# Performance work log

Measured on AMD Instinct MI355X. Metric: run time of the kernel, lower is better.

The kernel has to match this reference:

```python
import jax, jax.numpy as jnp
import numpy as np

B, P, Q, H = 8, 2048, 512, 1024


def setup_inputs() -> dict:
    key = jax.random.key(0)
    k1, k2, k3, k4, k5 = jax.random.split(key, 5)
    passage = jax.random.normal(k1, (B, P, H), dtype=jnp.float32)
    question = jax.random.normal(k2, (B, Q, H), dtype=jnp.float32)
    q_mask = jax.random.randint(k3, (B, Q), 0, 2, dtype=jnp.int32)
    # map_linear params (torch Linear: y = x @ W.T + b)
    bound = 1.0 / np.sqrt(H)
    map_W = jax.random.uniform(k4, (H, H), jnp.float32, -bound, bound)
    map_b = jax.random.uniform(k5, (H,), jnp.float32, -bound, bound)
    return {"passage": passage, "question": question, "q_mask": q_mask,
            "map_W": map_W, "map_b": map_b}


def reference(passage, question, q_mask, map_W, map_b):
    # scores: [B, P, Q]
    scores = jnp.einsum("bph,bqh->bpq", passage, question)
    mask = q_mask.astype(scores.dtype)[:, None, :]  # [B, 1, Q], broadcasts over P
    # multiplicative masked softmax + renormalize (memory_efficient=False path)
    a = jax.nn.softmax(scores * mask, axis=-1) * mask
    alpha = a / (jnp.sum(a, axis=-1, keepdims=True) + 1e-13)
    # attend: [B, P, H]
    out = jnp.einsum("bpq,bqh->bph", alpha, question)
    # fused linear + ReLU
    return jax.nn.relu(jnp.einsum("bph,oh->bpo", out, map_W) + map_b)
```

## Files before the change

kernel.cpp:

```cpp
#include <hip/hip_runtime.h>
#include <hip/hip_bf16.h>

typedef _Float16 f16;
typedef _Float16 f16x8 __attribute__((ext_vector_type(8)));
typedef _Float16 f16x4 __attribute__((ext_vector_type(4)));
typedef _Float16 f16x2 __attribute__((ext_vector_type(2)));
typedef float f32x4 __attribute__((ext_vector_type(4)));
typedef float f32x2 __attribute__((ext_vector_type(2)));

#define B_ 8
#define P_ 2048
#define Q_ 512
#define H_ 1024

__device__ __forceinline__ void gload_lds16(const void* g, void* l) {
  __builtin_amdgcn_global_load_lds(
      (const __attribute__((address_space(1))) void*)g,
      (__attribute__((address_space(3))) void*)l, 16, 0, 0);
}

__global__ __launch_bounds__(256) void k_cvt16(const float* __restrict__ x,
                                               f16* __restrict__ y, int n4) {
  int i = blockIdx.x * blockDim.x + threadIdx.x;
  int stride = gridDim.x * blockDim.x;
  for (; i < n4; i += stride) {
    f32x4 v = ((const f32x4*)x)[i];
    f16x4 h;
#pragma unroll
    for (int j = 0; j < 4; ++j) h[j] = (f16)v[j];
    ((f16x4*)y)[i] = h;
  }
}

__global__ __launch_bounds__(256) void k_transpose(const float* __restrict__ q,
                                                   f16* __restrict__ qT,
                                                   f16* __restrict__ q16) {
  __shared__ float t[64][65];
  int b = blockIdx.z;
  int h0 = blockIdx.x * 64, q0 = blockIdx.y * 64;
  int tid = threadIdx.x;
  int c4 = (tid & 15) * 4;
  int r16 = tid >> 4;
  const float* src = q + ((long)b * Q_ + q0) * H_ + h0;
  f16* d16 = q16 + ((long)b * Q_ + q0) * H_ + h0;
#pragma unroll
  for (int i = 0; i < 4; ++i) {
    int r = r16 + i * 16;
    f32x4 v = *(const f32x4*)(src + (long)r * H_ + c4);
    f16x4 s;
#pragma unroll
    for (int j = 0; j < 4; ++j) s[j] = (f16)v[j];
    *(f16x4*)(d16 + (long)r * H_ + c4) = s;
    t[c4 + 0][r] = v[0];
    t[c4 + 1][r] = v[1];
    t[c4 + 2][r] = v[2];
    t[c4 + 3][r] = v[3];
  }
  __syncthreads();
  f16* dst = qT + ((long)b * H_ + h0) * Q_ + q0;
#pragma unroll
  for (int i = 0; i < 4; ++i) {
    int hr = r16 + i * 16;
    f16x4 o;
#pragma unroll
    for (int j = 0; j < 4; ++j) o[j] = (f16)t[hr][c4 + j];
    *(f16x4*)(dst + (long)hr * Q_ + c4) = o;
  }
}

__global__ __launch_bounds__(512, 2) void k_score_softmax(
    const float* __restrict__ passage, const f16* __restrict__ q16,
    const int* __restrict__ qmask, f16* __restrict__ alpha) {
  constexpr int NT = H_ / 32;
  __shared__ __align__(16) f16 smem[2048 + 32768];

  int orig = blockIdx.x;
  int z = orig & 7;
  int row0 = (orig >> 3) * 32;

  int tid = threadIdx.x, wv = tid >> 6, lane = tid & 63;
  int fr = lane & 15, kq = lane >> 4;
  int wc = wv * 64;
  int swz = (kq ^ ((fr >> 1) & 3)) * 8;

  int arow = tid >> 4;
  int acol2 = (tid & 15) * 2;
  const float* gA = passage + ((long)(z * P_ + row0 + arow)) * H_ + acol2;
  int aw = arow * 32 + ((acol2 >> 3) ^ ((arow >> 1) & 3)) * 8 + (acol2 & 7);

  const f16* gB = q16 + ((long)(z * Q_ + (tid >> 2))) * H_ +
                  (((tid & 3) ^ ((tid >> 3) & 3)) * 8);

  auto stageB = [&](int t) {
    const f16* g = gB + t * 32;
    f16* l = smem + 2048 + (t & 1) * 16384 + wv * 512;
#pragma unroll
    for (int p = 0; p < 4; ++p)
      gload_lds16(g + (long)p * 128 * H_, l + p * 4096);
  };
  auto writeA = [&](int t, f32x2 av) {
    f16x2 h;
    h[0] = (f16)av[0];
    h[1] = (f16)av[1];
    *(f16x2*)(smem + (t & 1) * 1024 + aw) = h;
  };

  f32x4 acc[2][4] = {};
  f32x2 areg0, areg1;

  areg0 = *(const f32x2*)gA;
  stageB(0);
  areg1 = *(const f32x2*)(gA + 32);
  writeA(0, areg0);
  asm volatile("s_waitcnt vmcnt(1) lgkmcnt(0)" ::: "memory");
  __builtin_amdgcn_s_barrier();
  __builtin_amdgcn_sched_barrier(0);

#pragma unroll 2
  for (int t = 0; t < NT; ++t) {
    if (t + 1 < NT) stageB(t + 1);
    f16x8 af[2], bf[4];
    const f16* Ab = smem + (t & 1) * 1024;
    const f16* Bb = smem + 2048 + (t & 1) * 16384;
#pragma unroll
    for (int m = 0; m < 2; ++m)
      af[m] = *(const f16x8*)(Ab + (m * 16 + fr) * 32 + swz);
#pragma unroll
    for (int n = 0; n < 4; ++n)
      bf[n] = *(const f16x8*)(Bb + (wc + n * 16 + fr) * 32 + swz);
    if (t + 1 < NT)
      writeA(t + 1, ((t + 1) & 1) ? areg1 : areg0);
    if (t + 2 < NT) {
      f32x2 a = *(const f32x2*)(gA + (t + 2) * 32);
      if ((t + 2) & 1) areg1 = a; else areg0 = a;
    }
    __builtin_amdgcn_s_setprio(1);
#pragma unroll
    for (int m = 0; m < 2; ++m)
#pragma unroll
      for (int n = 0; n < 4; ++n)
        acc[m][n] = __builtin_amdgcn_mfma_f32_16x16x32_f16(af[m], bf[n],
                                                           acc[m][n], 0, 0, 0);
    __builtin_amdgcn_s_setprio(0);
    if (t < NT - 2)
      asm volatile("s_waitcnt vmcnt(1) lgkmcnt(0)" ::: "memory");
    else if (t == NT - 2)
      asm volatile("s_waitcnt vmcnt(0) lgkmcnt(0)" ::: "memory");
    if (t < NT - 1) {
      __builtin_amdgcn_s_barrier();
      __builtin_amdgcn_sched_barrier(0);
    }
  }

  __syncthreads();
  float* red = (float*)smem;
  float* red2 = red + 256;
  const int* qm = qmask + z * Q_;
  float mk[4];
#pragma unroll
  for (int n = 0; n < 4; ++n) mk[n] = (float)qm[wc + n * 16 + fr];

  int rb = (lane >> 4) * 4;
  float rmax[2][4];
#pragma unroll
  for (int m = 0; m < 2; ++m)
#pragma unroll
    for (int j = 0; j < 4; ++j) {
      float v = acc[m][0][j] * mk[0];
#pragma unroll
      for (int n = 1; n < 4; ++n) v = fmaxf(v, acc[m][n][j] * mk[n]);
      v = fmaxf(v, __shfl_xor(v, 1, 64));
      v = fmaxf(v, __shfl_xor(v, 2, 64));
      v = fmaxf(v, __shfl_xor(v, 4, 64));
      v = fmaxf(v, __shfl_xor(v, 8, 64));
      if (fr == 0) red[(rb + m * 16 + j) * 8 + wv] = v;
    }
  __syncthreads();
#pragma unroll
  for (int m = 0; m < 2; ++m)
#pragma unroll
    for (int j = 0; j < 4; ++j) {
      int r = rb + m * 16 + j;
      float v = red[r * 8];
#pragma unroll
      for (int w = 1; w < 8; ++w) v = fmaxf(v, red[r * 8 + w]);
      rmax[m][j] = v;
    }
#pragma unroll
  for (int m = 0; m < 2; ++m)
#pragma unroll
    for (int j = 0; j < 4; ++j) {
      float zs = 0.f, ss = 0.f;
#pragma unroll
      for (int n = 0; n < 4; ++n) {
        float e = expf(acc[m][n][j] * mk[n] - rmax[m][j]);
        acc[m][n][j] = e;
        zs += e;
        ss += e * mk[n];
      }
      zs += __shfl_xor(zs, 1, 64); ss += __shfl_xor(ss, 1, 64);
      zs += __shfl_xor(zs, 2, 64); ss += __shfl_xor(ss, 2, 64);
      zs += __shfl_xor(zs, 4, 64); ss += __shfl_xor(ss, 4, 64);
      zs += __shfl_xor(zs, 8, 64); ss += __shfl_xor(ss, 8, 64);
      if (fr == 0) {
        red2[((rb + m * 16 + j) * 8 + wv) * 2] = zs;
        red2[((rb + m * 16 + j) * 8 + wv) * 2 + 1] = ss;
      }
    }
  __syncthreads();
  f16* ap = alpha + ((long)(z * P_ + row0)) * Q_;
#pragma unroll
  for (int m = 0; m < 2; ++m)
#pragma unroll
    for (int j = 0; j < 4; ++j) {
      int r = rb + m * 16 + j;
      float Z = 0.f, Sm = 0.f;
#pragma unroll
      for (int w = 0; w < 8; ++w) {
        Z += red2[(r * 8 + w) * 2];
        Sm += red2[(r * 8 + w) * 2 + 1];
      }
      float inv = 1.0f / (Sm + 1e-13f * Z);
#pragma unroll
      for (int n = 0; n < 4; ++n)
        ap[(long)r * Q_ + wc + n * 16 + fr] = (f16)(acc[m][n][j] * mk[n] * inv);
    }
}

template <int EPI, int NT>
__global__ __launch_bounds__(512, 2) void k_gemm256(
    const f16* __restrict__ A, const f16* __restrict__ Bm,
    void* __restrict__ Cv, const float* __restrict__ bias, int N, int gx,
    int gy, long sA, long sB, long sC) {
  constexpr int K = NT * 32;
  __shared__ __align__(16) f16 smem[65536];

  int nwg = gridDim.x;
  int orig = blockIdx.x;
  int wg = (orig & 7) * (nwg >> 3) + (orig >> 3);
  int bx = wg % gx;
  int tt = wg / gx;
  int by = tt % gy;
  int z = tt / gy;
  int row0 = by * 256, col0 = bx * 256;
  A += z * sA;
  Bm += z * sB;

  int tid = threadIdx.x, wv = tid >> 6, lane = tid & 63;

  bool isA = wv < 4;
  int u0 = (wv & 3) * 4;
  int srow = u0 * 16 + (lane >> 2);
  int sclog = ((lane & 3) ^ ((lane >> 3) & 3)) * 8;
  const f16* sbaseG = isA ? A + (long)(row0 + srow) * K + sclog
                          : Bm + (long)(col0 + srow) * K + sclog;
  int sbaseL = (isA ? 0 : 8192) + u0 * 512;

  auto stage = [&](int tile) {
    const f16* g = sbaseG + (long)tile * 32;
    f16* l = smem + (tile & 3) * 16384 + sbaseL;
#pragma unroll
    for (int j = 0; j < 4; ++j) gload_lds16(g + (long)j * 16 * K, l + j * 512);
  };

  int wr = (wv >> 2) * 128, wc = (wv & 3) * 64;
  int fr = lane & 15, kq = lane >> 4;
  int swz = (kq ^ ((fr >> 1) & 3)) * 8 + fr * 32;

  f32x4 acc[8][4] = {};
  auto compute = [&](int t) {
    const f16* bufA = smem + (t & 3) * 16384;
    const f16* bufB = bufA + 8192;
    f16x8 af[8], bfr[4];
#pragma unroll
    for (int m = 0; m < 8; ++m)
      af[m] = *(const f16x8*)(bufA + (wr + m * 16) * 32 + swz);
#pragma unroll
    for (int n = 0; n < 4; ++n)
      bfr[n] = *(const f16x8*)(bufB + (wc + n * 16) * 32 + swz);
#pragma unroll
    for (int m = 0; m < 8; ++m)
#pragma unroll
      for (int n = 0; n < 4; ++n)
        acc[m][n] = __builtin_amdgcn_mfma_f32_16x16x32_f16(af[m], bfr[n],
                                                           acc[m][n], 0, 0, 0);
  };

  stage(0);
  stage(1);
  stage(2);
  asm volatile("s_waitcnt vmcnt(8)" ::: "memory");
  __builtin_amdgcn_s_barrier();
  __builtin_amdgcn_sched_barrier(0);
  for (int t = 0; t < NT - 3; ++t) {
    stage(t + 3);
    compute(t);
    asm volatile("s_waitcnt vmcnt(8)" ::: "memory");
    __builtin_amdgcn_s_barrier();
    __builtin_amdgcn_sched_barrier(0);
  }
  compute(NT - 3);
  asm volatile("s_waitcnt vmcnt(4)" ::: "memory");
  __builtin_amdgcn_s_barrier();
  __builtin_amdgcn_sched_barrier(0);
  compute(NT - 2);
  asm volatile("s_waitcnt vmcnt(0)" ::: "memory");
  __builtin_amdgcn_s_barrier();
  __builtin_amdgcn_sched_barrier(0);
  compute(NT - 1);

  int r0 = row0 + wr + (lane >> 4) * 4;
  int c0 = col0 + wc + fr;
  if constexpr (EPI == 1) {
    f16* C = (f16*)Cv + z * sC;
#pragma unroll
    for (int m = 0; m < 8; ++m)
#pragma unroll
      for (int n = 0; n < 4; ++n)
#pragma unroll
        for (int j = 0; j < 4; ++j)
          C[(long)(r0 + m * 16 + j) * N + c0 + n * 16] = (f16)acc[m][n][j];
  } else {
    float* C = (float*)Cv;
#pragma unroll
    for (int n = 0; n < 4; ++n) {
      float bv = bias[c0 + n * 16];
#pragma unroll
      for (int m = 0; m < 8; ++m)
#pragma unroll
        for (int j = 0; j < 4; ++j) {
          float v = acc[m][n][j] + bv;
          C[(long)(r0 + m * 16 + j) * N + c0 + n * 16] = fmaxf(v, 0.f);
        }
    }
  }
}

extern "C" void kernel_launch(void* const* d_in, const int* in_sizes, int n_in,
                              void* d_out, int out_size, void* d_ws,
                              size_t ws_size, hipStream_t stream) {
  const float* passage = (const float*)d_in[0];
  const float* question = (const float*)d_in[1];
  const int* qmask = (const int*)d_in[2];
  const float* mapW = (const float*)d_in[3];
  const float* mapb = (const float*)d_in[4];

  char* ws = (char*)d_ws;
  size_t off = 0;
  auto alloc = [&](size_t bytes) {
    void* p = ws + off;
    off += (bytes + 255) & ~(size_t)255;
    return p;
  };
  f16* q16 = (f16*)alloc((size_t)B_ * Q_ * H_ * 2);
  f16* qT = (f16*)alloc((size_t)B_ * H_ * Q_ * 2);
  f16* w16 = (f16*)alloc((size_t)H_ * H_ * 2);
  f16* alpha = (f16*)alloc((size_t)B_ * P_ * Q_ * 2);
  f16* O = (f16*)alloc((size_t)B_ * P_ * H_ * 2);

  k_cvt16<<<512, 256, 0, stream>>>(mapW, w16, H_ * H_ / 4);
  k_transpose<<<dim3(H_ / 64, Q_ / 64, B_), 256, 0, stream>>>(question, qT,
                                                              q16);

  k_score_softmax<<<512, 512, 0, stream>>>(passage, q16, qmask, alpha);

  k_gemm256<1, Q_ / 32><<<256, 512, 0, stream>>>(
      alpha, qT, O, nullptr, H_, H_ / 256, P_ / 256, (long)P_ * Q_,
      (long)H_ * Q_, (long)P_ * H_);

  k_gemm256<2, H_ / 32><<<256, 512, 0, stream>>>(
      O, w16, d_out, mapb, H_, H_ / 256, (B_ * P_) / 256, 0, 0, 0);
}
```

Measured before the change: 121.6 us.

## Split score GEMM and softmax into separate kernels with larger 128x256 tiles

```diff
diff --git a/kernel.cpp b/kernel.cpp
--- a/kernel.cpp
+++ b/kernel.cpp
@@ -4,9 +4,8 @@
 typedef _Float16 f16;
 typedef _Float16 f16x8 __attribute__((ext_vector_type(8)));
 typedef _Float16 f16x4 __attribute__((ext_vector_type(4)));
-typedef _Float16 f16x2 __attribute__((ext_vector_type(2)));
 typedef float f32x4 __attribute__((ext_vector_type(4)));
-typedef float f32x2 __attribute__((ext_vector_type(2)));
+typedef int i32x4 __attribute__((ext_vector_type(4)));
 
 #define B_ 8
 #define P_ 2048
@@ -68,83 +67,97 @@
   }
 }
 
-__global__ __launch_bounds__(512, 2) void k_score_softmax(
+__global__ __launch_bounds__(512, 2) void k_gemm1(
     const float* __restrict__ passage, const f16* __restrict__ q16,
-    const int* __restrict__ qmask, f16* __restrict__ alpha) {
+    float* __restrict__ S) {
   constexpr int NT = H_ / 32;
-  __shared__ __align__(16) f16 smem[2048 + 32768];
+  __shared__ __align__(16) f16 smem[40960];
 
   int orig = blockIdx.x;
-  int z = orig & 7;
-  int row0 = (orig >> 3) * 32;
+  int wg = (orig & 7) * 32 + (orig >> 3);
+  int bx = wg & 1, by = (wg >> 1) & 15, z = wg >> 5;
+  int row0 = by * 128, col0 = bx * 256;
 
   int tid = threadIdx.x, wv = tid >> 6, lane = tid & 63;
   int fr = lane & 15, kq = lane >> 4;
-  int wc = wv * 64;
+  int wr = (wv >> 2) * 64, wc = (wv & 3) * 64;
   int swz = (kq ^ ((fr >> 1) & 3)) * 8;
 
-  int arow = tid >> 4;
-  int acol2 = (tid & 15) * 2;
-  const float* gA = passage + ((long)(z * P_ + row0 + arow)) * H_ + acol2;
-  int aw = arow * 32 + ((acol2 >> 3) ^ ((arow >> 1) & 3)) * 8 + (acol2 & 7);
-
-  const f16* gB = q16 + ((long)(z * Q_ + (tid >> 2))) * H_ +
+  int ar = tid >> 2, ac = tid & 3;
+  const float* gA = passage + ((long)(z * P_ + row0 + ar)) * H_ + ac * 8;
+  int aw = ar * 32 + ((ac ^ ((ar >> 1) & 3)) * 8);
+
+  const f16* gB = q16 + ((long)(z * Q_ + col0 + (tid >> 2))) * H_ +
                   (((tid & 3) ^ ((tid >> 3) & 3)) * 8);
 
   auto stageB = [&](int t) {
     const f16* g = gB + t * 32;
-    f16* l = smem + 2048 + (t & 1) * 16384 + wv * 512;
-#pragma unroll
-    for (int p = 0; p < 4; ++p)
-      gload_lds16(g + (long)p * 128 * H_, l + p * 4096);
-  };
-  auto writeA = [&](int t, f32x2 av) {
-    f16x2 h;
-    h[0] = (f16)av[0];
-    h[1] = (f16)av[1];
-    *(f16x2*)(smem + (t & 1) * 1024 + aw) = h;
-  };
-
-  f32x4 acc[2][4] = {};
-  f32x2 areg0, areg1;
-
-  areg0 = *(const f32x2*)gA;
+    f16* l = smem + 8192 + (t & 3) * 8192 + wv * 512;
+    gload_lds16(g, l);
+    gload_lds16(g + (long)128 * H_, l + 4096);
+  };
+  auto writeA = [&](int t, f32x4 lo, f32x4 hi) {
+    f16x8 h;
+#pragma unroll
+    for (int j = 0; j < 4; ++j) {
+      h[j] = (f16)lo[j];
+      h[4 + j] = (f16)hi[j];
+    }
+    *(f16x8*)(smem + (t & 1) * 4096 + aw) = h;
+  };
+
+  f32x4 acc[4][4] = {};
+  f32x4 a0lo, a0hi, a1lo, a1hi;
+
+  a0lo = *(const f32x4*)(gA);
+  a0hi = *(const f32x4*)(gA + 4);
+  a1lo = *(const f32x4*)(gA + 32);
+  a1hi = *(const f32x4*)(gA + 36);
   stageB(0);
-  areg1 = *(const f32x2*)(gA + 32);
-  writeA(0, areg0);
-  asm volatile("s_waitcnt vmcnt(1) lgkmcnt(0)" ::: "memory");
+  stageB(1);
+  stageB(2);
+  writeA(0, a0lo, a0hi);
+  asm volatile("s_waitcnt vmcnt(4) lgkmcnt(0)" ::: "memory");
   __builtin_amdgcn_s_barrier();
   __builtin_amdgcn_sched_barrier(0);
 
-#pragma unroll 2
+#pragma unroll 4
   for (int t = 0; t < NT; ++t) {
-    if (t + 1 < NT) stageB(t + 1);
-    f16x8 af[2], bf[4];
-    const f16* Ab = smem + (t & 1) * 1024;
-    const f16* Bb = smem + 2048 + (t & 1) * 16384;
-#pragma unroll
-    for (int m = 0; m < 2; ++m)
-      af[m] = *(const f16x8*)(Ab + (m * 16 + fr) * 32 + swz);
+    if (t + 2 < NT) {
+      const float* g = gA + (t + 2) * 32;
+      if (t & 1) {
+        a1lo = *(const f32x4*)(g);
+        a1hi = *(const f32x4*)(g + 4);
+      } else {
+        a0lo = *(const f32x4*)(g);
+        a0hi = *(const f32x4*)(g + 4);
+      }
+    }
+    if (t + 3 < NT) stageB(t + 3);
+    f16x8 af[4], bf[4];
+    const f16* Ab = smem + (t & 1) * 4096;
+    const f16* Bb = smem + 8192 + (t & 3) * 8192;
+#pragma unroll
+    for (int m = 0; m < 4; ++m)
+      af[m] = *(const f16x8*)(Ab + (wr + m * 16 + fr) * 32 + swz);
 #pragma unroll
     for (int n = 0; n < 4; ++n)
       bf[n] = *(const f16x8*)(Bb + (wc + n * 16 + fr) * 32 + swz);
     if (t + 1 < NT)
-      writeA(t + 1, ((t + 1) & 1) ? areg1 : areg0);
-    if (t + 2 < NT) {
-      f32x2 a = *(const f32x2*)(gA + (t + 2) * 32);
-      if ((t + 2) & 1) areg1 = a; else areg0 = a;
-    }
+      writeA(t + 1, (t & 1) ? a0lo : a1lo, (t & 1) ? a0hi : a1hi);
     __builtin_amdgcn_s_setprio(1);
 #pragma unroll
-    for (int m = 0; m < 2; ++m)
+    for (int m = 0; m < 4; ++m)
 #pragma unroll
       for (int n = 0; n < 4; ++n)
         acc[m][n] = __builtin_amdgcn_mfma_f32_16x16x32_f16(af[m], bf[n],
                                                            acc[m][n], 0, 0, 0);
     __builtin_amdgcn_s_setprio(0);
-    if (t < NT - 2)
-      asm volatile("s_waitcnt vmcnt(1) lgkmcnt(0)" ::: "memory");
-    else if (t == NT - 2)
+    if (t <= NT - 4)
+      asm volatile("s_waitcnt vmcnt(6) lgkmcnt(0)" ::: "memory");
+    else if (t == NT - 3)
+      asm volatile("s_waitcnt vmcnt(4) lgkmcnt(0)" ::: "memory");
+    else
       asm volatile("s_waitcnt vmcnt(0) lgkmcnt(0)" ::: "memory");
     if (t < NT - 1) {
       __builtin_amdgcn_s_barrier();
@@ -152,79 +165,56 @@
     }
   }
 
-  __syncthreads();
-  float* red = (float*)smem;
-  float* red2 = red + 256;
-  const int* qm = qmask + z * Q_;
-  float mk[4];
-#pragma unroll
-  for (int n = 0; n < 4; ++n) mk[n] = (float)qm[wc + n * 16 + fr];
-
-  int rb = (lane >> 4) * 4;
-  float rmax[2][4];
-#pragma unroll
-  for (int m = 0; m < 2; ++m)
-#pragma unroll
-    for (int j = 0; j < 4; ++j) {
-      float v = acc[m][0][j] * mk[0];
-#pragma unroll
-      for (int n = 1; n < 4; ++n) v = fmaxf(v, acc[m][n][j] * mk[n]);
-      v = fmaxf(v, __shfl_xor(v, 1, 64));
-      v = fmaxf(v, __shfl_xor(v, 2, 64));
-      v = fmaxf(v, __shfl_xor(v, 4, 64));
-      v = fmaxf(v, __shfl_xor(v, 8, 64));
-      if (fr == 0) red[(rb + m * 16 + j) * 8 + wv] = v;
-    }
-  __syncthreads();
-#pragma unroll
-  for (int m = 0; m < 2; ++m)
-#pragma unroll
-    for (int j = 0; j < 4; ++j) {
-      int r = rb + m * 16 + j;
-      float v = red[r * 8];
-#pragma unroll
-      for (int w = 1; w < 8; ++w) v = fmaxf(v, red[r * 8 + w]);
-      rmax[m][j] = v;
-    }
-#pragma unroll
-  for (int m = 0; m < 2; ++m)
-#pragma unroll
-    for (int j = 0; j < 4; ++j) {
-      float zs = 0.f, ss = 0.f;
-#pragma unroll
-      for (int n = 0; n < 4; ++n) {
-        float e = expf(acc[m][n][j] * mk[n] - rmax[m][j]);
-        acc[m][n][j] = e;
-        zs += e;
-        ss += e * mk[n];
-      }
-      zs += __shfl_xor(zs, 1, 64); ss += __shfl_xor(ss, 1, 64);
-      zs += __shfl_xor(zs, 2, 64); ss += __shfl_xor(ss, 2, 64);
-      zs += __shfl_xor(zs, 4, 64); ss += __shfl_xor(ss, 4, 64);
-      zs += __shfl_xor(zs, 8, 64); ss += __shfl_xor(ss, 8, 64);
-      if (fr == 0) {
-        red2[((rb + m * 16 + j) * 8 + wv) * 2] = zs;
-        red2[((rb + m * 16 + j) * 8 + wv) * 2 + 1] = ss;
-      }
-    }
-  __syncthreads();
-  f16* ap = alpha + ((long)(z * P_ + row0)) * Q_;
-#pragma unroll
-  for (int m = 0; m < 2; ++m)
-#pragma unroll
-    for (int j = 0; j < 4; ++j) {
-      int r = rb + m * 16 + j;
-      float Z = 0.f, Sm = 0.f;
-#pragma unroll
-      for (int w = 0; w < 8; ++w) {
-        Z += red2[(r * 8 + w) * 2];
-        Sm += red2[(r * 8 + w) * 2 + 1];
-      }
-      float inv = 1.0f / (Sm + 1e-13f * Z);
-#pragma unroll
-      for (int n = 0; n < 4; ++n)
-        ap[(long)r * Q_ + wc + n * 16 + fr] = (f16)(acc[m][n][j] * mk[n] * inv);
-    }
+  float* Sp = S + (long)z * P_ * Q_;
+  int r0 = row0 + wr + (lane >> 4) * 4;
+  int c0 = col0 + wc + fr;
+#pragma unroll
+  for (int m = 0; m < 4; ++m)
+#pragma unroll
+    for (int n = 0; n < 4; ++n)
+#pragma unroll
+      for (int j = 0; j < 4; ++j)
+        Sp[(long)(r0 + m * 16 + j) * Q_ + c0 + n * 16] = acc[m][n][j];
+}
+
+__global__ __launch_bounds__(256) void k_softmax(const float* __restrict__ S,
+                                                 const int* __restrict__ qmask,
+                                                 f16* __restrict__ alpha) {
+  int row = blockIdx.x * 4 + (threadIdx.x >> 6);
+  int lane = threadIdx.x & 63;
+  int b = row >> 11;
+  const float* s = S + (long)row * Q_;
+  const int* mp = qmask + b * Q_;
+  f32x4 v0 = ((const f32x4*)s)[lane * 2];
+  f32x4 v1 = ((const f32x4*)s)[lane * 2 + 1];
+  i32x4 m0 = ((const i32x4*)mp)[lane * 2];
+  i32x4 m1 = ((const i32x4*)mp)[lane * 2 + 1];
+  float t[8], mf[8];
+#pragma unroll
+  for (int j = 0; j < 4; ++j) {
+    mf[j] = (float)m0[j];     t[j] = v0[j] * mf[j];
+    mf[4 + j] = (float)m1[j]; t[4 + j] = v1[j] * mf[4 + j];
+  }
+  float mx = t[0];
+#pragma unroll
+  for (int j = 1; j < 8; ++j) mx = fmaxf(mx, t[j]);
+  for (int o = 32; o; o >>= 1) mx = fmaxf(mx, __shfl_xor(mx, o, 64));
+  float e[8], Z = 0.f, Sm = 0.f;
+#pragma unroll
+  for (int j = 0; j < 8; ++j) {
+    e[j] = expf(t[j] - mx);
+    Z += e[j];
+    Sm += e[j] * mf[j];
+  }
+  for (int o = 32; o; o >>= 1) {
+    Z += __shfl_xor(Z, o, 64);
+    Sm += __shfl_xor(Sm, o, 64);
+  }
+  float inv = 1.0f / (Sm + 1e-13f * Z);
+  f16x8 out;
+#pragma unroll
+  for (int j = 0; j < 8; ++j) out[j] = (f16)(e[j] * mf[j] * inv);
+  *(f16x8*)(alpha + (long)row * Q_ + lane * 8) = out;
 }
 
 template <int EPI, int NT>
@@ -357,12 +347,15 @@
   f16* w16 = (f16*)alloc((size_t)H_ * H_ * 2);
   f16* alpha = (f16*)alloc((size_t)B_ * P_ * Q_ * 2);
   f16* O = (f16*)alloc((size_t)B_ * P_ * H_ * 2);
+  float* S = (float*)alloc((size_t)B_ * P_ * Q_ * 4);
 
   k_cvt16<<<512, 256, 0, stream>>>(mapW, w16, H_ * H_ / 4);
   k_transpose<<<dim3(H_ / 64, Q_ / 64, B_), 256, 0, stream>>>(question, qT,
                                                               q16);
 
-  k_score_softmax<<<512, 512, 0, stream>>>(passage, q16, qmask, alpha);
+  k_gemm1<<<256, 512, 0, stream>>>(passage, q16, S);
+
+  k_softmax<<<B_ * P_ / 4, 256, 0, stream>>>(S, qmask, alpha);
 
   k_gemm256<1, Q_ / 32><<<256, 512, 0, stream>>>(
       alpha, qT, O, nullptr, H_, H_ / 256, P_ / 256, (long)P_ * Q_,
```

Result: no change. 123.5 us, median of 2 (+1.5%).
